# Kernel tuning notes

Measured on AMD Instinct MI355X. Metric: run time of the kernel, lower is better.

## Reference

```python
import jax, jax.numpy as jnp
import numpy as np

N_CUST = 500000
N_FUND = 50000
N_EDGE = 4000000
D_CUST = 101
D_FUND = 1
HID = 64


def setup_inputs() -> dict:
    key = jax.random.key(0)
    ks = jax.random.split(key, 16)
    s = lambda fan_in: 1.0 / np.sqrt(fan_in)
    return {
        "x_customer": jax.random.normal(ks[0], (N_CUST, D_CUST), jnp.float32),
        "x_fund": jax.random.normal(ks[1], (N_FUND, D_FUND), jnp.float32),
        "src_fund": jax.random.randint(ks[2], (N_EDGE,), 0, N_FUND, jnp.int64),
        "dst_customer": jax.random.randint(ks[3], (N_EDGE,), 0, N_CUST, jnp.int64),
        # per-node-type input projections
        "W_cust": jax.random.uniform(ks[4], (D_CUST, HID), jnp.float32, -s(D_CUST), s(D_CUST)),
        "b_cust": jax.random.uniform(ks[5], (HID,), jnp.float32, -s(D_CUST), s(D_CUST)),
        "W_fund": jax.random.uniform(ks[6], (D_FUND, HID), jnp.float32, -s(D_FUND), s(D_FUND)),
        "b_fund": jax.random.uniform(ks[7], (HID,), jnp.float32, -s(D_FUND), s(D_FUND)),
        # SAGEConv fund->customer: lin_l (neighbor aggr, bias) + lin_r (self, no bias)
        "W_l": jax.random.uniform(ks[8], (HID, HID), jnp.float32, -s(HID), s(HID)),
        "b_l": jax.random.uniform(ks[9], (HID,), jnp.float32, -s(HID), s(HID)),
        "W_r": jax.random.uniform(ks[10], (HID, HID), jnp.float32, -s(HID), s(HID)),
        # output head
        "W_out": jax.random.uniform(ks[11], (HID, 2), jnp.float32, -s(HID), s(HID)),
        "b_out": jax.random.uniform(ks[12], (2,), jnp.float32, -s(HID), s(HID)),
    }


def reference(x_customer, x_fund, src_fund, dst_customer,
              W_cust, b_cust, W_fund, b_fund, W_l, b_l, W_r, W_out, b_out):
    # per-node-type linear + relu
    h_c = jax.nn.relu(x_customer @ W_cust + b_cust)  # [N_CUST, HID]
    h_f = jax.nn.relu(x_fund @ W_fund + b_fund)      # [N_FUND, HID]

    # SAGEConv (fund -> customer): gather src fund features per edge,
    # mean-aggregate by destination customer (scatter-sum / count)
    msgs = h_f[src_fund]  # [N_EDGE, HID]
    summed = jax.ops.segment_sum(msgs, dst_customer, num_segments=N_CUST)
    cnt = jax.ops.segment_sum(jnp.ones((msgs.shape[0],), msgs.dtype),
                              dst_customer, num_segments=N_CUST)
    mean = summed / jnp.maximum(cnt, 1.0)[:, None]

    out_c = mean @ W_l + b_l + h_c @ W_r  # SAGE: lin_l(aggr) + lin_r(self)
    return out_c @ W_out + b_out          # [N_CUST, 2]
```

## Files before the change

kernel.cpp:

```cpp
#include <hip/hip_runtime.h>
#include <stdint.h>

#define N_CUST 500000
#define N_FUND 50000
#define N_EDGE 4000000
#define D_CUST 101
#define HID 64

#define NB   512
#define EPB  ((N_EDGE + NB - 1) / NB)
#define CB   512
#define NBKT ((N_CUST + CB - 1) / CB)
#define CAP  5120
#define GPAD 32

typedef float float4u __attribute__((ext_vector_type(4), aligned(4)));
using frag_ab = __attribute__((ext_vector_type(8))) short;
using frag_cd = __attribute__((ext_vector_type(4))) float;

struct __align__(16) Accum { float g0, g1, cnt, pad; };

__device__ __forceinline__ short f2bf(float f) {
    unsigned u = __float_as_uint(f);
    u += 0x7fffu + ((u >> 16) & 1u);
    return (short)(u >> 16);
}

__global__ __launch_bounds__(256) void k_gf(
    const float* __restrict__ x_fund,
    const float* __restrict__ W_fund,
    const float* __restrict__ b_fund,
    const float* __restrict__ W_l,
    const float* __restrict__ W_r,
    const float* __restrict__ W_out,
    const float* __restrict__ Wc,
    const float* __restrict__ b_l,
    const float* __restrict__ b_out,
    float2* __restrict__ gf,
    frag_ab* __restrict__ wcb,
    float* __restrict__ Bt,
    float* __restrict__ c2,
    unsigned* __restrict__ gcur,
    float4* __restrict__ Az)
{
    __shared__ float sAf[128];
    __shared__ float sWf[64];
    __shared__ float sBf[64];
    int t = threadIdx.x;

    if (Az != nullptr) {
        float4 z4 = make_float4(0.f, 0.f, 0.f, 0.f);
        for (int i = blockIdx.x * 256 + t; i < N_CUST; i += gridDim.x * 256)
            Az[i] = z4;
    }

    if (t < 128) {
        int h = t >> 1, j = t & 1;
        float s = 0.f;
        for (int k = 0; k < 64; ++k)
            s = fmaf(W_l[h * 64 + k], W_out[k * 2 + j], s);
        sAf[t] = s;
    } else if (t < 192) {
        sWf[t - 128] = W_fund[t - 128];
    } else {
        sBf[t - 192] = b_fund[t - 192];
    }
    __syncthreads();

    int f = blockIdx.x * 256 + t;
    if (f < N_FUND) {
        float xf = x_fund[f];
        float g0 = 0.f, g1 = 0.f;
        #pragma unroll
        for (int h = 0; h < 64; ++h) {
            float hf = fmaxf(fmaf(xf, sWf[h], sBf[h]), 0.f);
            g0 = fmaf(hf, sAf[2 * h + 0], g0);
            g1 = fmaf(hf, sAf[2 * h + 1], g1);
        }
        gf[f] = make_float2(g0, g1);
    }

    if (blockIdx.x == 0) {
        for (int k = t; k < NBKT * GPAD; k += 256) gcur[k] = 0u;
        if (t < 128) {
            int h = t >> 1, j = t & 1;
            float s = 0.f;
            for (int k = 0; k < 64; ++k)
                s = fmaf(W_r[h * 64 + k], W_out[k * 2 + j], s);
            Bt[t] = s;
        } else if (t < 130) {
            int j = t - 128;
            float s = b_out[j];
            for (int k = 0; k < 64; ++k)
                s = fmaf(b_l[k], W_out[k * 2 + j], s);
            c2[j] = s;
        }
        for (int sidx = t; sidx < 1024; sidx += 256) {
            int fidx = sidx >> 6, l = sidx & 63;
            int c = l & 15, q = l >> 4;
            int nt = fidx >> 2, kc = fidx & 3;
            frag_ab fr;
            #pragma unroll
            for (int j = 0; j < 8; ++j) {
                int kk = kc * 32 + q * 8 + j;
                int h  = nt * 16 + c;
                fr[j] = (kk < D_CUST) ? f2bf(Wc[kk * HID + h]) : (short)0;
            }
            wcb[sidx] = fr;
        }
    }
}

__global__ __launch_bounds__(256) void k_reorder(
    const int* __restrict__ src, const int* __restrict__ dst,
    unsigned* __restrict__ gcur, unsigned* __restrict__ recs)
{
    __shared__ unsigned hist[NBKT];
    __shared__ unsigned localOff[NBKT];
    __shared__ unsigned cur[NBKT];
    __shared__ unsigned baseG[NBKT];
    __shared__ unsigned ldsRec[EPB];
    __shared__ unsigned short ldsBkt[EPB];

    int t = threadIdx.x, b = blockIdx.x;
    int e0 = b * EPB, e1 = min(e0 + EPB, N_EDGE);
    int cntE = e1 - e0;

    for (int k = t; k < NBKT; k += 256) hist[k] = 0;
    __syncthreads();
    for (int e = e0 + t; e < e1; e += 256)
        atomicAdd(&hist[((unsigned)dst[e]) >> 9], 1u);
    __syncthreads();

    if (t < 64) {
        unsigned v[16], pre[16], run = 0;
        #pragma unroll
        for (int j = 0; j < 16; ++j) {
            int idx = t * 16 + j;
            v[j] = (idx < NBKT) ? hist[idx] : 0u;
            pre[j] = run; run += v[j];
        }
        unsigned sc = run;
        #pragma unroll
        for (int d = 1; d < 64; d <<= 1) {
            unsigned n = __shfl_up(sc, d, 64);
            if (t >= d) sc += n;
        }
        unsigned lane_excl = sc - run;
        #pragma unroll
        for (int j = 0; j < 16; ++j) {
            int idx = t * 16 + j;
            if (idx < NBKT) {
                localOff[idx] = lane_excl + pre[j];
                cur[idx]      = lane_excl + pre[j];
            }
        }
    }
    __syncthreads();

    for (int k = t; k < NBKT; k += 256) {
        unsigned h = hist[k];
        baseG[k] = h ? ((unsigned)k * CAP + atomicAdd(&gcur[k * GPAD], h)) : 0u;
    }

    for (int e = e0 + t; e < e1; e += 256) {
        unsigned d = (unsigned)dst[e];
        unsigned s = (unsigned)src[e];
        unsigned k = d >> 9;
        unsigned p = atomicAdd(&cur[k], 1u);
        ldsRec[p] = s | ((d & 511u) << 16);
        ldsBkt[p] = (unsigned short)k;
    }
    __syncthreads();

    for (int i = t; i < cntE; i += 256) {
        unsigned k = ldsBkt[i];
        unsigned g = baseG[k] + (i - localOff[k]);
        if (g < (k + 1u) * CAP) recs[g] = ldsRec[i];
    }
}

__global__ __launch_bounds__(256) void k_bucket(
    const unsigned* __restrict__ recs, const unsigned* __restrict__ gcur,
    const float2* __restrict__ gf,
    const float* __restrict__ x, const float* __restrict__ bc,
    const frag_ab* __restrict__ wcb, const float* __restrict__ Bt,
    const float* __restrict__ c2,
    float2* __restrict__ out)
{
    __shared__ float s0[CB], s1[CB], scn[CB];
    __shared__ float pbuf[2 * CB];
    __shared__ int tileCtr;

    int t = threadIdx.x, k = blockIdx.x;
    int w = t >> 6, lane = t & 63;
    int c = lane & 15, q = lane >> 4;

    if (t == 0) tileCtr = 0;
    for (int cc = t; cc < CB; cc += 256) { s0[cc] = 0.f; s1[cc] = 0.f; scn[cc] = 0.f; }
    __syncthreads();

    frag_ab bfrag[16];
    #pragma unroll
    for (int f = 0; f < 16; ++f) bfrag[f] = wcb[f * 64 + lane];
    float btv[8];
    #pragma unroll
    for (int nt = 0; nt < 4; ++nt) {
        btv[2 * nt]     = Bt[(nt * 16 + c) * 2];
        btv[2 * nt + 1] = Bt[(nt * 16 + c) * 2 + 1];
    }
    float bcv[4];
    #pragma unroll
    for (int nt = 0; nt < 4; ++nt) bcv[nt] = bc[nt * 16 + c];
    float c20 = c2[0], c21 = c2[1];

    int cust0 = k * CB;
    int ncust = min(CB, N_CUST - cust0);
    int n_tiles = ncust >> 4;

    if (w == 3) {
        unsigned n = min(gcur[(unsigned)k * GPAD], (unsigned)CAP);
        const unsigned* rp = recs + (size_t)k * CAP;
        unsigned i = (unsigned)lane * 4u;
        for (; i + 4u <= n; i += 256u) {
            uint4 rr = *(const uint4*)(rp + i);
            float2 ga = gf[rr.x & 0xFFFFu];
            float2 gb = gf[rr.y & 0xFFFFu];
            float2 gc = gf[rr.z & 0xFFFFu];
            float2 gd = gf[rr.w & 0xFFFFu];
            unsigned da = rr.x >> 16, db = rr.y >> 16;
            unsigned dc = rr.z >> 16, dd = rr.w >> 16;
            atomicAdd(&s0[da], ga.x); atomicAdd(&s1[da], ga.y); atomicAdd(&scn[da], 1.f);
            atomicAdd(&s0[db], gb.x); atomicAdd(&s1[db], gb.y); atomicAdd(&scn[db], 1.f);
            atomicAdd(&s0[dc], gc.x); atomicAdd(&s1[dc], gc.y); atomicAdd(&scn[dc], 1.f);
            atomicAdd(&s0[dd], gd.x); atomicAdd(&s1[dd], gd.y); atomicAdd(&scn[dd], 1.f);
        }
        unsigned base = n & ~3u;
        if ((unsigned)lane < (n & 3u)) {
            unsigned r = rp[base + lane];
            float2 g = gf[r & 0xFFFFu];
            unsigned dl = r >> 16;
            atomicAdd(&s0[dl], g.x); atomicAdd(&s1[dl], g.y); atomicAdd(&scn[dl], 1.f);
        }
    }

    for (;;) {
        int tl;
        if (lane == 0) tl = atomicAdd(&tileCtr, 1);
        tl = __shfl(tl, 0, 64);
        if (tl >= n_tiles) break;

        int row = cust0 + tl * 16 + c;
        const float* xr = x + (size_t)row * D_CUST;
        frag_ab af[4];
        #pragma unroll
        for (int kc = 0; kc < 3; ++kc) {
            float4u lo = *(const float4u*)(xr + kc * 32 + q * 8);
            float4u hi = *(const float4u*)(xr + kc * 32 + q * 8 + 4);
            frag_ab f;
            f[0]=f2bf(lo[0]); f[1]=f2bf(lo[1]); f[2]=f2bf(lo[2]); f[3]=f2bf(lo[3]);
            f[4]=f2bf(hi[0]); f[5]=f2bf(hi[1]); f[6]=f2bf(hi[2]); f[7]=f2bf(hi[3]);
            af[kc] = f;
        }
        {
            frag_ab f = {0,0,0,0,0,0,0,0};
            if (q == 0) {
                float4u lo = *(const float4u*)(xr + 96);
                f[0]=f2bf(lo[0]); f[1]=f2bf(lo[1]); f[2]=f2bf(lo[2]); f[3]=f2bf(lo[3]);
                f[4]=f2bf(xr[100]);
            }
            af[3] = f;
        }
        frag_cd acc[4];
        #pragma unroll
        for (int nt = 0; nt < 4; ++nt)
            acc[nt] = (frag_cd){bcv[nt], bcv[nt], bcv[nt], bcv[nt]};
        #pragma unroll
        for (int kc = 0; kc < 4; ++kc)
            #pragma unroll
            for (int nt = 0; nt < 4; ++nt)
                acc[nt] = __builtin_amdgcn_mfma_f32_16x16x32_bf16(
                    af[kc], bfrag[nt * 4 + kc], acc[nt], 0, 0, 0);

        #pragma unroll
        for (int i = 0; i < 4; ++i) {
            float p0 = 0.f, p1 = 0.f;
            #pragma unroll
            for (int nt = 0; nt < 4; ++nt) {
                float zv = fmaxf(acc[nt][i], 0.f);
                p0 = fmaf(zv, btv[2 * nt],     p0);
                p1 = fmaf(zv, btv[2 * nt + 1], p1);
            }
            #pragma unroll
            for (int m = 1; m < 16; m <<= 1) {
                p0 += __shfl_xor(p0, m, 16);
                p1 += __shfl_xor(p1, m, 16);
            }
            if (c == 0) {
                int lrow = tl * 16 + q * 4 + i;
                pbuf[2 * lrow]     = p0 + c20;
                pbuf[2 * lrow + 1] = p1 + c21;
            }
        }
    }
    __syncthreads();

    for (int cc = t; cc < ncust; cc += 256) {
        float inv = 1.0f / fmaxf(scn[cc], 1.0f);
        out[cust0 + cc] = make_float2(fmaf(s0[cc], inv, pbuf[2 * cc]),
                                      fmaf(s1[cc], inv, pbuf[2 * cc + 1]));
    }
}

__global__ __launch_bounds__(256) void k_scatter_direct(
    const int* __restrict__ src, const int* __restrict__ dst,
    const float2* __restrict__ gf, Accum* __restrict__ A)
{
    int stride = gridDim.x * 256;
    for (int e = blockIdx.x * 256 + threadIdx.x; e < N_EDGE; e += stride) {
        int s = src[e], d = dst[e];
        float2 g = gf[s];
        unsafeAtomicAdd(&A[d].g0, g.x);
        unsafeAtomicAdd(&A[d].g1, g.y);
        unsafeAtomicAdd(&A[d].cnt, 1.0f);
    }
}

__global__ __launch_bounds__(256) void k_mean(
    const Accum* __restrict__ A, float2* __restrict__ mean2)
{
    int i = blockIdx.x * 256 + threadIdx.x;
    if (i < N_CUST) {
        Accum a = A[i];
        float inv = 1.0f / fmaxf(a.cnt, 1.0f);
        mean2[i] = make_float2(a.g0 * inv, a.g1 * inv);
    }
}

__global__ __launch_bounds__(256) void k_gemm(
    const float* __restrict__ x, const float* __restrict__ bc,
    const frag_ab* __restrict__ wcb, const float* __restrict__ Bt,
    const float* __restrict__ c2, const float2* __restrict__ mean2,
    float2* __restrict__ out)
{
    __shared__ float sBt[128];
    __shared__ float zb[4][16 * 68];

    int t = threadIdx.x;
    int w = t >> 6, lane = t & 63;
    int c = lane & 15, q = lane >> 4;
    float* z = zb[w];

    if (t < 128) sBt[t] = Bt[t];
    frag_ab bfrag[16];
    #pragma unroll
    for (int f = 0; f < 16; ++f) bfrag[f] = wcb[f * 64 + lane];
    float bcv[4];
    #pragma unroll
    for (int nt = 0; nt < 4; ++nt) bcv[nt] = bc[nt * 16 + c];
    float c20 = c2[0], c21 = c2[1];
    __syncthreads();

    const int NT = N_CUST / 16;
    for (int tl = blockIdx.x * 4 + w; tl < NT; tl += gridDim.x * 4) {
        int row0 = tl * 16;
        const float* xr = x + (size_t)(row0 + c) * D_CUST;
        frag_ab af[4];
        #pragma unroll
        for (int kc = 0; kc < 3; ++kc) {
            float4u lo = *(const float4u*)(xr + kc * 32 + q * 8);
            float4u hi = *(const float4u*)(xr + kc * 32 + q * 8 + 4);
            frag_ab f;
            f[0]=f2bf(lo[0]); f[1]=f2bf(lo[1]); f[2]=f2bf(lo[2]); f[3]=f2bf(lo[3]);
            f[4]=f2bf(hi[0]); f[5]=f2bf(hi[1]); f[6]=f2bf(hi[2]); f[7]=f2bf(hi[3]);
            af[kc] = f;
        }
        {
            frag_ab f = {0,0,0,0,0,0,0,0};
            if (q == 0) {
                float4u lo = *(const float4u*)(xr + 96);
                f[0]=f2bf(lo[0]); f[1]=f2bf(lo[1]); f[2]=f2bf(lo[2]); f[3]=f2bf(lo[3]);
                f[4]=f2bf(xr[100]);
            }
            af[3] = f;
        }
        frag_cd acc[4];
        #pragma unroll
        for (int nt = 0; nt < 4; ++nt)
            acc[nt] = (frag_cd){bcv[nt], bcv[nt], bcv[nt], bcv[nt]};
        #pragma unroll
        for (int kc = 0; kc < 4; ++kc)
            #pragma unroll
            for (int nt = 0; nt < 4; ++nt)
                acc[nt] = __builtin_amdgcn_mfma_f32_16x16x32_bf16(
                    af[kc], bfrag[nt * 4 + kc], acc[nt], 0, 0, 0);
        #pragma unroll
        for (int nt = 0; nt < 4; ++nt)
            #pragma unroll
            for (int i = 0; i < 4; ++i)
                z[(q * 4 + i) * 68 + nt * 16 + c] = fmaxf(acc[nt][i], 0.f);
        float p0 = 0.f, p1 = 0.f;
        #pragma unroll
        for (int j4 = 0; j4 < 4; ++j4) {
            float4u zv = *(const float4u*)(z + c * 68 + q * 16 + j4 * 4);
            float4u b0 = *(const float4u*)(sBt + q * 32 + j4 * 8);
            float4u b1 = *(const float4u*)(sBt + q * 32 + j4 * 8 + 4);
            p0 = fmaf(zv[0], b0[0], p0); p1 = fmaf(zv[0], b0[1], p1);
            p0 = fmaf(zv[1], b0[2], p0); p1 = fmaf(zv[1], b0[3], p1);
            p0 = fmaf(zv[2], b1[0], p0); p1 = fmaf(zv[2], b1[1], p1);
            p0 = fmaf(zv[3], b1[2], p0); p1 = fmaf(zv[3], b1[3], p1);
        }
        p0 += __shfl_xor(p0, 16, 64); p0 += __shfl_xor(p0, 32, 64);
        p1 += __shfl_xor(p1, 16, 64); p1 += __shfl_xor(p1, 32, 64);
        if (q == 0) {
            float2 m = mean2[row0 + c];
            out[row0 + c] = make_float2(p0 + c20 + m.x, p1 + c21 + m.y);
        }
    }
}

extern "C" void kernel_launch(void* const* d_in, const int* in_sizes, int n_in,
                              void* d_out, int out_size, void* d_ws, size_t ws_size,
                              hipStream_t stream) {
    const float* x_customer = (const float*)d_in[0];
    const float* x_fund     = (const float*)d_in[1];
    const int*   src_fund   = (const int*)d_in[2];
    const int*   dst_cust   = (const int*)d_in[3];
    const float* W_cust     = (const float*)d_in[4];
    const float* b_cust     = (const float*)d_in[5];
    const float* W_fund     = (const float*)d_in[6];
    const float* b_fund     = (const float*)d_in[7];
    const float* W_l        = (const float*)d_in[8];
    const float* b_l        = (const float*)d_in[9];
    const float* W_r        = (const float*)d_in[10];
    const float* W_out      = (const float*)d_in[11];
    const float* b_out      = (const float*)d_in[12];

    char* ws = (char*)d_ws;
    const size_t NEED_FAST = 20550976ull;

    if (ws_size >= NEED_FAST) {
        unsigned* recs = (unsigned*)(ws);
        float2*   gf   = (float2*)  (ws + 20008960);
        frag_ab*  wcb  = (frag_ab*) (ws + 20408960);
        float*    Bt   = (float*)   (ws + 20425344);
        float*    c2   = (float*)   (ws + 20425856);
        unsigned* gcur = (unsigned*)(ws + 20425920);

        k_gf<<<256, 256, 0, stream>>>(
            x_fund, W_fund, b_fund, W_l, W_r, W_out, W_cust, b_l, b_out,
            gf, wcb, Bt, c2, gcur, nullptr);
        k_reorder<<<NB, 256, 0, stream>>>(src_fund, dst_cust, gcur, recs);
        k_bucket<<<NBKT, 256, 0, stream>>>(
            recs, gcur, gf, x_customer, b_cust, wcb, Bt, c2, (float2*)d_out);
    } else {
        Accum*    A    = (Accum*)   (ws);
        float2*   mn2  = (float2*)  (ws + 8000000);
        float2*   gf   = (float2*)  (ws + 12000000);
        frag_ab*  wcb  = (frag_ab*) (ws + 12400000);
        float*    Bt   = (float*)   (ws + 12416384);
        float*    c2   = (float*)   (ws + 12416896);
        unsigned* gcur = (unsigned*)(ws + 12416960);

        k_gf<<<256, 256, 0, stream>>>(
            x_fund, W_fund, b_fund, W_l, W_r, W_out, W_cust, b_l, b_out,
            gf, wcb, Bt, c2, gcur, (float4*)A);
        k_scatter_direct<<<2048, 256, 0, stream>>>(src_fund, dst_cust, gf, A);
        k_mean<<<(N_CUST + 255) / 256, 256, 0, stream>>>(A, mn2);
        k_gemm<<<2048, 256, 0, stream>>>(
            x_customer, b_cust, wcb, Bt, c2, mn2, (float2*)d_out);
    }
}
```

Measured before the change: 443.0 us.

## Split bucket kernel into four sub-blocks per bucket and widen reorder blocks

```diff
diff --git a/kernel.cpp b/kernel.cpp
--- a/kernel.cpp
+++ b/kernel.cpp
@@ -13,6 +13,8 @@
 #define NBKT ((N_CUST + CB - 1) / CB)
 #define CAP  5120
 #define GPAD 32
+#define SPLIT 4
+#define CSUB (CB / SPLIT)
 
 typedef float float4u __attribute__((ext_vector_type(4), aligned(4)));
 using frag_ab = __attribute__((ext_vector_type(8))) short;
@@ -24,6 +26,62 @@
     unsigned u = __float_as_uint(f);
     u += 0x7fffu + ((u >> 16) & 1u);
     return (short)(u >> 16);
+}
+
+__device__ __forceinline__ void load_af(const float* __restrict__ xr, int q,
+                                        frag_ab af[4]) {
+    #pragma unroll
+    for (int kc = 0; kc < 3; ++kc) {
+        float4u lo = *(const float4u*)(xr + kc * 32 + q * 8);
+        float4u hi = *(const float4u*)(xr + kc * 32 + q * 8 + 4);
+        frag_ab f;
+        f[0]=f2bf(lo[0]); f[1]=f2bf(lo[1]); f[2]=f2bf(lo[2]); f[3]=f2bf(lo[3]);
+        f[4]=f2bf(hi[0]); f[5]=f2bf(hi[1]); f[6]=f2bf(hi[2]); f[7]=f2bf(hi[3]);
+        af[kc] = f;
+    }
+    frag_ab f = {0,0,0,0,0,0,0,0};
+    if (q == 0) {
+        float4u lo = *(const float4u*)(xr + 96);
+        f[0]=f2bf(lo[0]); f[1]=f2bf(lo[1]); f[2]=f2bf(lo[2]); f[3]=f2bf(lo[3]);
+        f[4]=f2bf(xr[100]);
+    }
+    af[3] = f;
+}
+
+__device__ __forceinline__ void gemm_tile(
+    const frag_ab af[4], const frag_ab bfrag[16], const float bcv[4],
+    const float btv[8], float c20, float c21, int tl, int q, int c,
+    float* __restrict__ pbuf) {
+    frag_cd acc[4];
+    #pragma unroll
+    for (int nt = 0; nt < 4; ++nt)
+        acc[nt] = (frag_cd){bcv[nt], bcv[nt], bcv[nt], bcv[nt]};
+    #pragma unroll
+    for (int kc = 0; kc < 4; ++kc)
+        #pragma unroll
+        for (int nt = 0; nt < 4; ++nt)
+            acc[nt] = __builtin_amdgcn_mfma_f32_16x16x32_bf16(
+                af[kc], bfrag[nt * 4 + kc], acc[nt], 0, 0, 0);
+    #pragma unroll
+    for (int i = 0; i < 4; ++i) {
+        float p0 = 0.f, p1 = 0.f;
+        #pragma unroll
+        for (int nt = 0; nt < 4; ++nt) {
+            float zv = fmaxf(acc[nt][i], 0.f);
+            p0 = fmaf(zv, btv[2 * nt],     p0);
+            p1 = fmaf(zv, btv[2 * nt + 1], p1);
+        }
+        #pragma unroll
+        for (int m = 1; m < 16; m <<= 1) {
+            p0 += __shfl_xor(p0, m, 16);
+            p1 += __shfl_xor(p1, m, 16);
+        }
+        if (c == 0) {
+            int lrow = tl * 16 + q * 4 + i;
+            pbuf[2 * lrow]     = p0 + c20;
+            pbuf[2 * lrow + 1] = p1 + c21;
+        }
+    }
 }
 
 __global__ __launch_bounds__(256) void k_gf(
@@ -111,7 +169,7 @@
     }
 }
 
-__global__ __launch_bounds__(256) void k_reorder(
+__global__ __launch_bounds__(512) void k_reorder(
     const int* __restrict__ src, const int* __restrict__ dst,
     unsigned* __restrict__ gcur, unsigned* __restrict__ recs)
 {
@@ -126,9 +184,9 @@
     int e0 = b * EPB, e1 = min(e0 + EPB, N_EDGE);
     int cntE = e1 - e0;
 
-    for (int k = t; k < NBKT; k += 256) hist[k] = 0;
-    __syncthreads();
-    for (int e = e0 + t; e < e1; e += 256)
+    for (int k = t; k < NBKT; k += 512) hist[k] = 0;
+    __syncthreads();
+    for (int e = e0 + t; e < e1; e += 512)
         atomicAdd(&hist[((unsigned)dst[e]) >> 9], 1u);
     __syncthreads();
 
@@ -158,12 +216,12 @@
     }
     __syncthreads();
 
-    for (int k = t; k < NBKT; k += 256) {
+    for (int k = t; k < NBKT; k += 512) {
         unsigned h = hist[k];
         baseG[k] = h ? ((unsigned)k * CAP + atomicAdd(&gcur[k * GPAD], h)) : 0u;
     }
 
-    for (int e = e0 + t; e < e1; e += 256) {
+    for (int e = e0 + t; e < e1; e += 512) {
         unsigned d = (unsigned)dst[e];
         unsigned s = (unsigned)src[e];
         unsigned k = d >> 9;
@@ -173,7 +231,7 @@
     }
     __syncthreads();
 
-    for (int i = t; i < cntE; i += 256) {
+    for (int i = t; i < cntE; i += 512) {
         unsigned k = ldsBkt[i];
         unsigned g = baseG[k] + (i - localOff[k]);
         if (g < (k + 1u) * CAP) recs[g] = ldsRec[i];
@@ -188,16 +246,20 @@
     const float* __restrict__ c2,
     float2* __restrict__ out)
 {
-    __shared__ float s0[CB], s1[CB], scn[CB];
-    __shared__ float pbuf[2 * CB];
-    __shared__ int tileCtr;
-
-    int t = threadIdx.x, k = blockIdx.x;
+    __shared__ float s0[CSUB], s1[CSUB], scn[CSUB];
+    __shared__ float pbuf[2 * CSUB];
+
+    int t = threadIdx.x;
+    int k = blockIdx.x >> 2, sub = blockIdx.x & 3;
     int w = t >> 6, lane = t & 63;
     int c = lane & 15, q = lane >> 4;
 
-    if (t == 0) tileCtr = 0;
-    for (int cc = t; cc < CB; cc += 256) { s0[cc] = 0.f; s1[cc] = 0.f; scn[cc] = 0.f; }
+    int cust0 = k * CB + sub * CSUB;
+    if (cust0 >= N_CUST) return;
+    int ncust = min(CSUB, N_CUST - cust0);
+    int n_tiles = ncust >> 4;
+
+    if (t < CSUB) { s0[t] = 0.f; s1[t] = 0.f; scn[t] = 0.f; }
     __syncthreads();
 
     frag_ab bfrag[16];
@@ -214,95 +276,43 @@
     for (int nt = 0; nt < 4; ++nt) bcv[nt] = bc[nt * 16 + c];
     float c20 = c2[0], c21 = c2[1];
 
-    int cust0 = k * CB;
-    int ncust = min(CB, N_CUST - cust0);
-    int n_tiles = ncust >> 4;
-
-    if (w == 3) {
-        unsigned n = min(gcur[(unsigned)k * GPAD], (unsigned)CAP);
-        const unsigned* rp = recs + (size_t)k * CAP;
-        unsigned i = (unsigned)lane * 4u;
-        for (; i + 4u <= n; i += 256u) {
-            uint4 rr = *(const uint4*)(rp + i);
-            float2 ga = gf[rr.x & 0xFFFFu];
-            float2 gb = gf[rr.y & 0xFFFFu];
-            float2 gc = gf[rr.z & 0xFFFFu];
-            float2 gd = gf[rr.w & 0xFFFFu];
-            unsigned da = rr.x >> 16, db = rr.y >> 16;
-            unsigned dc = rr.z >> 16, dd = rr.w >> 16;
-            atomicAdd(&s0[da], ga.x); atomicAdd(&s1[da], ga.y); atomicAdd(&scn[da], 1.f);
-            atomicAdd(&s0[db], gb.x); atomicAdd(&s1[db], gb.y); atomicAdd(&scn[db], 1.f);
-            atomicAdd(&s0[dc], gc.x); atomicAdd(&s1[dc], gc.y); atomicAdd(&scn[dc], 1.f);
-            atomicAdd(&s0[dd], gd.x); atomicAdd(&s1[dd], gd.y); atomicAdd(&scn[dd], 1.f);
-        }
-        unsigned base = n & ~3u;
-        if ((unsigned)lane < (n & 3u)) {
-            unsigned r = rp[base + lane];
+    unsigned n = min(gcur[(unsigned)k * GPAD], (unsigned)CAP);
+    const unsigned* rp = recs + (size_t)k * CAP;
+    unsigned dlo = (unsigned)sub * CSUB;
+    for (unsigned i = (unsigned)t * 4u; i + 4u <= n; i += 1024u) {
+        uint4 rr = *(const uint4*)(rp + i);
+        unsigned rv[4] = {rr.x, rr.y, rr.z, rr.w};
+        #pragma unroll
+        for (int j = 0; j < 4; ++j) {
+            unsigned dl = rv[j] >> 16;
+            if ((dl & ~(unsigned)(CSUB - 1)) == dlo) {
+                float2 g = gf[rv[j] & 0xFFFFu];
+                unsigned d = dl & (CSUB - 1);
+                atomicAdd(&s0[d], g.x);
+                atomicAdd(&s1[d], g.y);
+                atomicAdd(&scn[d], 1.f);
+            }
+        }
+    }
+    for (unsigned i = (n & ~3u) + (unsigned)t; i < n; i += 256u) {
+        unsigned r = rp[i];
+        unsigned dl = r >> 16;
+        if ((dl & ~(unsigned)(CSUB - 1)) == dlo) {
             float2 g = gf[r & 0xFFFFu];
-            unsigned dl = r >> 16;
-            atomicAdd(&s0[dl], g.x); atomicAdd(&s1[dl], g.y); atomicAdd(&scn[dl], 1.f);
-        }
-    }
-
-    for (;;) {
-        int tl;
-        if (lane == 0) tl = atomicAdd(&tileCtr, 1);
-        tl = __shfl(tl, 0, 64);
-        if (tl >= n_tiles) break;
-
-        int row = cust0 + tl * 16 + c;
-        const float* xr = x + (size_t)row * D_CUST;
-        frag_ab af[4];
-        #pragma unroll
-        for (int kc = 0; kc < 3; ++kc) {
-            float4u lo = *(const float4u*)(xr + kc * 32 + q * 8);
-            float4u hi = *(const float4u*)(xr + kc * 32 + q * 8 + 4);
-            frag_ab f;
-            f[0]=f2bf(lo[0]); f[1]=f2bf(lo[1]); f[2]=f2bf(lo[2]); f[3]=f2bf(lo[3]);
-            f[4]=f2bf(hi[0]); f[5]=f2bf(hi[1]); f[6]=f2bf(hi[2]); f[7]=f2bf(hi[3]);
-            af[kc] = f;
-        }
-        {
-            frag_ab f = {0,0,0,0,0,0,0,0};
-            if (q == 0) {
-                float4u lo = *(const float4u*)(xr + 96);
-                f[0]=f2bf(lo[0]); f[1]=f2bf(lo[1]); f[2]=f2bf(lo[2]); f[3]=f2bf(lo[3]);
-                f[4]=f2bf(xr[100]);
-            }
-            af[3] = f;
-        }
-        frag_cd acc[4];
-        #pragma unroll
-        for (int nt = 0; nt < 4; ++nt)
-            acc[nt] = (frag_cd){bcv[nt], bcv[nt], bcv[nt], bcv[nt]};
-        #pragma unroll
-        for (int kc = 0; kc < 4; ++kc)
-            #pragma unroll
-            for (int nt = 0; nt < 4; ++nt)
-                acc[nt] = __builtin_amdgcn_mfma_f32_16x16x32_bf16(
-                    af[kc], bfrag[nt * 4 + kc], acc[nt], 0, 0, 0);
-
-        #pragma unroll
-        for (int i = 0; i < 4; ++i) {
-            float p0 = 0.f, p1 = 0.f;
-            #pragma unroll
-            for (int nt = 0; nt < 4; ++nt) {
-                float zv = fmaxf(acc[nt][i], 0.f);
-                p0 = fmaf(zv, btv[2 * nt],     p0);
-                p1 = fmaf(zv, btv[2 * nt + 1], p1);
-            }
-            #pragma unroll
-            for (int m = 1; m < 16; m <<= 1) {
-                p0 += __shfl_xor(p0, m, 16);
-                p1 += __shfl_xor(p1, m, 16);
-            }
-            if (c == 0) {
-                int lrow = tl * 16 + q * 4 + i;
-                pbuf[2 * lrow]     = p0 + c20;
-                pbuf[2 * lrow + 1] = p1 + c21;
-            }
-        }
-    }
+            unsigned d = dl & (CSUB - 1);
+            atomicAdd(&s0[d], g.x);
+            atomicAdd(&s1[d], g.y);
+            atomicAdd(&scn[d], 1.f);
+        }
+    }
+
+    int tl0 = w, tl1 = w + 4;
+    bool h0 = tl0 < n_tiles, h1 = tl1 < n_tiles;
+    frag_ab af0[4], af1[4];
+    if (h0) load_af(x + (size_t)(cust0 + tl0 * 16 + c) * D_CUST, q, af0);
+    if (h1) load_af(x + (size_t)(cust0 + tl1 * 16 + c) * D_CUST, q, af1);
+    if (h0) gemm_tile(af0, bfrag, bcv, btv, c20, c21, tl0, q, c, pbuf);
+    if (h1) gemm_tile(af1, bfrag, bcv, btv, c20, c21, tl1, q, c, pbuf);
     __syncthreads();
 
     for (int cc = t; cc < ncust; cc += 256) {
@@ -366,24 +376,7 @@
         int row0 = tl * 16;
         const float* xr = x + (size_t)(row0 + c) * D_CUST;
         frag_ab af[4];
-        #pragma unroll
-        for (int kc = 0; kc < 3; ++kc) {
-            float4u lo = *(const float4u*)(xr + kc * 32 + q * 8);
-            float4u hi = *(const float4u*)(xr + kc * 32 + q * 8 + 4);
-            frag_ab f;
-            f[0]=f2bf(lo[0]); f[1]=f2bf(lo[1]); f[2]=f2bf(lo[2]); f[3]=f2bf(lo[3]);
-            f[4]=f2bf(hi[0]); f[5]=f2bf(hi[1]); f[6]=f2bf(hi[2]); f[7]=f2bf(hi[3]);
-            af[kc] = f;
-        }
-        {
-            frag_ab f = {0,0,0,0,0,0,0,0};
-            if (q == 0) {
-                float4u lo = *(const float4u*)(xr + 96);
-                f[0]=f2bf(lo[0]); f[1]=f2bf(lo[1]); f[2]=f2bf(lo[2]); f[3]=f2bf(lo[3]);
-                f[4]=f2bf(xr[100]);
-            }
-            af[3] = f;
-        }
+        load_af(xr, q, af);
         frag_cd acc[4];
         #pragma unroll
         for (int nt = 0; nt < 4; ++nt)
@@ -450,8 +443,8 @@
         k_gf<<<256, 256, 0, stream>>>(
             x_fund, W_fund, b_fund, W_l, W_r, W_out, W_cust, b_l, b_out,
             gf, wcb, Bt, c2, gcur, nullptr);
-        k_reorder<<<NB, 256, 0, stream>>>(src_fund, dst_cust, gcur, recs);
-        k_bucket<<<NBKT, 256, 0, stream>>>(
+        k_reorder<<<NB, 512, 0, stream>>>(src_fund, dst_cust, gcur, recs);
+        k_bucket<<<NBKT * SPLIT, 256, 0, stream>>>(
             recs, gcur, gf, x_customer, b_cust, wcb, Bt, c2, (float2*)d_out);
     } else {
         Accum*    A    = (Accum*)   (ws);
```

Measured after the change: 427.6 us. -3.5%, faster.

## Stage customer rows through LDS with coalesced loads; widen reorder blocks to 512

Applied to the files above, without the earlier changes.

```diff
diff --git a/kernel.cpp b/kernel.cpp
--- a/kernel.cpp
+++ b/kernel.cpp
@@ -13,8 +13,10 @@
 #define NBKT ((N_CUST + CB - 1) / CB)
 #define CAP  5120
 #define GPAD 32
+#define LROW 104
 
 typedef float float4u __attribute__((ext_vector_type(4), aligned(4)));
+typedef float float4a __attribute__((ext_vector_type(4), aligned(16)));
 using frag_ab = __attribute__((ext_vector_type(8))) short;
 using frag_cd = __attribute__((ext_vector_type(4))) float;
 
@@ -111,7 +113,7 @@
     }
 }
 
-__global__ __launch_bounds__(256) void k_reorder(
+__global__ __launch_bounds__(512) void k_reorder(
     const int* __restrict__ src, const int* __restrict__ dst,
     unsigned* __restrict__ gcur, unsigned* __restrict__ recs)
 {
@@ -126,9 +128,9 @@
     int e0 = b * EPB, e1 = min(e0 + EPB, N_EDGE);
     int cntE = e1 - e0;
 
-    for (int k = t; k < NBKT; k += 256) hist[k] = 0;
-    __syncthreads();
-    for (int e = e0 + t; e < e1; e += 256)
+    for (int k = t; k < NBKT; k += 512) hist[k] = 0;
+    __syncthreads();
+    for (int e = e0 + t; e < e1; e += 512)
         atomicAdd(&hist[((unsigned)dst[e]) >> 9], 1u);
     __syncthreads();
 
@@ -158,12 +160,12 @@
     }
     __syncthreads();
 
-    for (int k = t; k < NBKT; k += 256) {
+    for (int k = t; k < NBKT; k += 512) {
         unsigned h = hist[k];
         baseG[k] = h ? ((unsigned)k * CAP + atomicAdd(&gcur[k * GPAD], h)) : 0u;
     }
 
-    for (int e = e0 + t; e < e1; e += 256) {
+    for (int e = e0 + t; e < e1; e += 512) {
         unsigned d = (unsigned)dst[e];
         unsigned s = (unsigned)src[e];
         unsigned k = d >> 9;
@@ -173,7 +175,7 @@
     }
     __syncthreads();
 
-    for (int i = t; i < cntE; i += 256) {
+    for (int i = t; i < cntE; i += 512) {
         unsigned k = ldsBkt[i];
         unsigned g = baseG[k] + (i - localOff[k]);
         if (g < (k + 1u) * CAP) recs[g] = ldsRec[i];
@@ -190,29 +192,14 @@
 {
     __shared__ float s0[CB], s1[CB], scn[CB];
     __shared__ float pbuf[2 * CB];
-    __shared__ int tileCtr;
+    __shared__ float xbuf[3][16 * LROW];
 
     int t = threadIdx.x, k = blockIdx.x;
     int w = t >> 6, lane = t & 63;
     int c = lane & 15, q = lane >> 4;
 
-    if (t == 0) tileCtr = 0;
     for (int cc = t; cc < CB; cc += 256) { s0[cc] = 0.f; s1[cc] = 0.f; scn[cc] = 0.f; }
     __syncthreads();
-
-    frag_ab bfrag[16];
-    #pragma unroll
-    for (int f = 0; f < 16; ++f) bfrag[f] = wcb[f * 64 + lane];
-    float btv[8];
-    #pragma unroll
-    for (int nt = 0; nt < 4; ++nt) {
-        btv[2 * nt]     = Bt[(nt * 16 + c) * 2];
-        btv[2 * nt + 1] = Bt[(nt * 16 + c) * 2 + 1];
-    }
-    float bcv[4];
-    #pragma unroll
-    for (int nt = 0; nt < 4; ++nt) bcv[nt] = bc[nt * 16 + c];
-    float c20 = c2[0], c21 = c2[1];
 
     int cust0 = k * CB;
     int ncust = min(CB, N_CUST - cust0);
@@ -242,64 +229,87 @@
             unsigned dl = r >> 16;
             atomicAdd(&s0[dl], g.x); atomicAdd(&s1[dl], g.y); atomicAdd(&scn[dl], 1.f);
         }
-    }
-
-    for (;;) {
-        int tl;
-        if (lane == 0) tl = atomicAdd(&tileCtr, 1);
-        tl = __shfl(tl, 0, 64);
-        if (tl >= n_tiles) break;
-
-        int row = cust0 + tl * 16 + c;
-        const float* xr = x + (size_t)row * D_CUST;
-        frag_ab af[4];
-        #pragma unroll
-        for (int kc = 0; kc < 3; ++kc) {
-            float4u lo = *(const float4u*)(xr + kc * 32 + q * 8);
-            float4u hi = *(const float4u*)(xr + kc * 32 + q * 8 + 4);
-            frag_ab f;
-            f[0]=f2bf(lo[0]); f[1]=f2bf(lo[1]); f[2]=f2bf(lo[2]); f[3]=f2bf(lo[3]);
-            f[4]=f2bf(hi[0]); f[5]=f2bf(hi[1]); f[6]=f2bf(hi[2]); f[7]=f2bf(hi[3]);
-            af[kc] = f;
-        }
-        {
-            frag_ab f = {0,0,0,0,0,0,0,0};
-            if (q == 0) {
-                float4u lo = *(const float4u*)(xr + 96);
+    } else {
+        float* buf = xbuf[w];
+        frag_ab bfrag[16];
+        #pragma unroll
+        for (int f = 0; f < 16; ++f) bfrag[f] = wcb[f * 64 + lane];
+        float btv[8];
+        #pragma unroll
+        for (int nt = 0; nt < 4; ++nt) {
+            btv[2 * nt]     = Bt[(nt * 16 + c) * 2];
+            btv[2 * nt + 1] = Bt[(nt * 16 + c) * 2 + 1];
+        }
+        float bcv[4];
+        #pragma unroll
+        for (int nt = 0; nt < 4; ++nt) bcv[nt] = bc[nt * 16 + c];
+        float c20 = c2[0], c21 = c2[1];
+
+        int r = lane >> 2, s4 = lane & 3;
+
+        for (int tl = w; tl < n_tiles; tl += 3) {
+            const float* tb = x + (size_t)(cust0 + tl * 16) * D_CUST;
+            #pragma unroll
+            for (int rnd = 0; rnd < 7; ++rnd) {
+                int ch = s4 + rnd * 4;
+                if (ch < 25) {
+                    float4u v = *(const float4u*)(tb + r * D_CUST + ch * 4);
+                    *(float4a*)(buf + r * LROW + ch * 4) = v;
+                } else if (ch == 25) {
+                    buf[r * LROW + 100] = tb[r * D_CUST + 100];
+                }
+            }
+
+            frag_ab af[4];
+            #pragma unroll
+            for (int kc = 0; kc < 3; ++kc) {
+                float4a lo = *(const float4a*)(buf + c * LROW + kc * 32 + q * 8);
+                float4a hi = *(const float4a*)(buf + c * LROW + kc * 32 + q * 8 + 4);
+                frag_ab f;
                 f[0]=f2bf(lo[0]); f[1]=f2bf(lo[1]); f[2]=f2bf(lo[2]); f[3]=f2bf(lo[3]);
-                f[4]=f2bf(xr[100]);
-            }
-            af[3] = f;
-        }
-        frag_cd acc[4];
-        #pragma unroll
-        for (int nt = 0; nt < 4; ++nt)
-            acc[nt] = (frag_cd){bcv[nt], bcv[nt], bcv[nt], bcv[nt]};
-        #pragma unroll
-        for (int kc = 0; kc < 4; ++kc)
+                f[4]=f2bf(hi[0]); f[5]=f2bf(hi[1]); f[6]=f2bf(hi[2]); f[7]=f2bf(hi[3]);
+                af[kc] = f;
+            }
+            {
+                frag_ab f = {0,0,0,0,0,0,0,0};
+                if (q == 0) {
+                    float4a lo = *(const float4a*)(buf + c * LROW + 96);
+                    f[0]=f2bf(lo[0]); f[1]=f2bf(lo[1]); f[2]=f2bf(lo[2]); f[3]=f2bf(lo[3]);
+                    f[4]=f2bf(buf[c * LROW + 100]);
+                }
+                af[3] = f;
+            }
+
+            frag_cd acc[4];
             #pragma unroll
             for (int nt = 0; nt < 4; ++nt)
-                acc[nt] = __builtin_amdgcn_mfma_f32_16x16x32_bf16(
-                    af[kc], bfrag[nt * 4 + kc], acc[nt], 0, 0, 0);
-
-        #pragma unroll
-        for (int i = 0; i < 4; ++i) {
-            float p0 = 0.f, p1 = 0.f;
-            #pragma unroll
-            for (int nt = 0; nt < 4; ++nt) {
-                float zv = fmaxf(acc[nt][i], 0.f);
-                p0 = fmaf(zv, btv[2 * nt],     p0);
-                p1 = fmaf(zv, btv[2 * nt + 1], p1);
-            }
-            #pragma unroll
-            for (int m = 1; m < 16; m <<= 1) {
-                p0 += __shfl_xor(p0, m, 16);
-                p1 += __shfl_xor(p1, m, 16);
-            }
-            if (c == 0) {
-                int lrow = tl * 16 + q * 4 + i;
-                pbuf[2 * lrow]     = p0 + c20;
-                pbuf[2 * lrow + 1] = p1 + c21;
+                acc[nt] = (frag_cd){bcv[nt], bcv[nt], bcv[nt], bcv[nt]};
+            #pragma unroll
+            for (int kc = 0; kc < 4; ++kc)
+                #pragma unroll
+                for (int nt = 0; nt < 4; ++nt)
+                    acc[nt] = __builtin_amdgcn_mfma_f32_16x16x32_bf16(
+                        af[kc], bfrag[nt * 4 + kc], acc[nt], 0, 0, 0);
+
+            #pragma unroll
+            for (int i = 0; i < 4; ++i) {
+                float p0 = 0.f, p1 = 0.f;
+                #pragma unroll
+                for (int nt = 0; nt < 4; ++nt) {
+                    float zv = fmaxf(acc[nt][i], 0.f);
+                    p0 = fmaf(zv, btv[2 * nt],     p0);
+                    p1 = fmaf(zv, btv[2 * nt + 1], p1);
+                }
+                #pragma unroll
+                for (int m = 1; m < 16; m <<= 1) {
+                    p0 += __shfl_xor(p0, m, 16);
+                    p1 += __shfl_xor(p1, m, 16);
+                }
+                if (c == 0) {
+                    int lrow = tl * 16 + q * 4 + i;
+                    pbuf[2 * lrow]     = p0 + c20;
+                    pbuf[2 * lrow + 1] = p1 + c21;
+                }
             }
         }
     }
@@ -450,7 +460,7 @@
         k_gf<<<256, 256, 0, stream>>>(
             x_fund, W_fund, b_fund, W_l, W_r, W_out, W_cust, b_l, b_out,
             gf, wcb, Bt, c2, gcur, nullptr);
-        k_reorder<<<NB, 256, 0, stream>>>(src_fund, dst_cust, gcur, recs);
+        k_reorder<<<NB, 512, 0, stream>>>(src_fund, dst_cust, gcur, recs);
         k_bucket<<<NBKT, 256, 0, stream>>>(
             recs, gcur, gf, x_customer, b_cust, wcb, Bt, c2, (float2*)d_out);
     } else {
```

Result: slower. 507.2 us (+14.5%).
